# Optimization experiments

Hardware: AMD Instinct MI355X
Metric: run time of the kernel (lower is better)

The kernel has to match this reference:

```python
import jax, jax.numpy as jnp
import numpy as np

# Fixed by module source / config defaults
L, H, D, DFF, T, B = 4, 4, 128, 512, 64, 1024
S, V, BOS = 4, 5, 4            # 4 orbital states, vocab 5, BOS token id 4
DH = D // H


def _ln(x, w, b):
    mu = x.mean(-1, keepdims=True)
    var = ((x - mu) ** 2).mean(-1, keepdims=True)
    return (x - mu) / jnp.sqrt(var + 1e-5) * w + b


def _decode(gumbel, state_emb, pos_emb, ln1_w, ln1_b, wqkv, bqkv, wo, bo,
            ln2_w, ln2_b, w1, b1, w2, b2, fn_w, fn_b, head_w, head_b,
            n_alpha, n_beta):
    def step(carry, xs):
        tok, a_rem, b_rem, Kc, Vc = carry
        g, i = xs                                   # g: (B,4), i: step index
        x = state_emb[tok] + pos_emb[i]             # (B, D)
        for l in range(L):
            # pre-LN causal self-attention with KV cache (torch MHA math)
            xn = _ln(x, ln1_w[l], ln1_b[l])
            q, k, v = jnp.split(xn @ wqkv[l].T + bqkv[l], 3, axis=-1)
            Kc = Kc.at[l, :, i].set(k)
            Vc = Vc.at[l, :, i].set(v)
            qh = q.reshape(B, H, DH)
            kh = Kc[l].reshape(B, T, H, DH)
            vh = Vc[l].reshape(B, T, H, DH)
            sc = jnp.einsum('bhd,bthd->bht', qh, kh) / jnp.sqrt(jnp.float32(DH))
            sc = jnp.where((jnp.arange(T) <= i)[None, None, :], sc, -jnp.inf)
            ctx = jnp.einsum('bht,bthd->bhd', jax.nn.softmax(sc, -1), vh).reshape(B, D)
            x = x + ctx @ wo[l].T + bo[l]
            # pre-LN FFN (exact GELU, matching nn.GELU default)
            h = jax.nn.gelu(_ln(x, ln2_w[l], ln2_b[l]) @ w1[l].T + b1[l], approximate=False)
            x = x + h @ w2[l].T + b2[l]
        logits = _ln(x, fn_w, fn_b) @ head_w.T + head_b   # (B, 4)
        # electron-budget validity mask (compute_validity_mask)
        oa = T - i - 1
        m = jnp.stack([
            (a_rem <= oa) & (b_rem <= oa),
            (b_rem > 0) & (a_rem <= oa) & (b_rem - 1 <= oa),
            (a_rem > 0) & (a_rem - 1 <= oa) & (b_rem <= oa),
            (a_rem > 0) & (b_rem > 0) & (a_rem - 1 <= oa) & (b_rem - 1 <= oa)], -1)
        logp = jax.nn.log_softmax(jnp.where(m, logits, -jnp.inf), -1)
        s = jnp.argmax(logp + g, -1)                # gumbel-max == multinomial
        lp = jnp.take_along_axis(logp, s[:, None], 1)[:, 0]
        return (s, a_rem - (s >> 1), b_rem - (s & 1), Kc, Vc), (s, lp)

    tok0 = jnp.full((B,), BOS, jnp.int32)
    a0 = jnp.full((B,), n_alpha, jnp.int32)
    b0 = jnp.full((B,), n_beta, jnp.int32)
    Kc0 = jnp.zeros((L, B, T, D), jnp.float32)
    Vc0 = jnp.zeros((L, B, T, D), jnp.float32)
    _, (states, lps) = jax.lax.scan(
        step, (tok0, a0, b0, Kc0, Vc0), (gumbel.transpose(1, 0, 2), jnp.arange(T)))
    return states.T, lps.sum(0)                      # (B, T) states, (B,) log-prob


def setup_inputs() -> dict:
    key = jax.random.key(0)
    ks = jax.random.split(key, 10)
    p = lambda k, shp: jax.random.normal(k, shp, jnp.float32) * 0.02
    u = jax.random.uniform(ks[0], (B, T, S), jnp.float32, 1e-6, 1.0 - 1e-6)
    return {
        'gumbel': -jnp.log(-jnp.log(u)),
        'state_emb': p(ks[1], (V, D)),
        'pos_emb': p(ks[2], (T + 1, D)),
        'ln1_w': jnp.ones((L, D)), 'ln1_b': jnp.zeros((L, D)),
        'wqkv': p(ks[3], (L, 3 * D, D)), 'bqkv': jnp.zeros((L, 3 * D)),
        'wo': p(ks[4], (L, D, D)), 'bo': jnp.zeros((L, D)),
        'ln2_w': jnp.ones((L, D)), 'ln2_b': jnp.zeros((L, D)),
        'w1': p(ks[5], (L, DFF, D)), 'b1': jnp.zeros((L, DFF)),
        'w2': p(ks[6], (L, D, DFF)), 'b2': jnp.zeros((L, D)),
        'fn_w': jnp.ones((D,)), 'fn_b': jnp.zeros((D,)),
        'head_w': p(ks[7], (S, D)), 'head_b': jnp.zeros((S,)),
        'n_alpha': 16, 'n_beta': 16,
    }


def reference(gumbel, state_emb, pos_emb, ln1_w, ln1_b, wqkv, bqkv, wo, bo,
              ln2_w, ln2_b, w1, b1, w2, b2, fn_w, fn_b, head_w, head_b,
              n_alpha, n_beta):
    return _decode(gumbel, state_emb, pos_emb, ln1_w, ln1_b, wqkv, bqkv, wo, bo,
                   ln2_w, ln2_b, w1, b1, w2, b2, fn_w, fn_b, head_w, head_b,
                   n_alpha, n_beta)
```

## Files before the change

### kernel.cpp

```cpp
#include <hip/hip_runtime.h>
#include <math.h>

namespace {
constexpr int L_ = 4, H_ = 4, D_ = 128, DFF_ = 512, T_ = 64, B_ = 1024;
constexpr int S_ = 4, BOS_ = 4, DH_ = 32;
constexpr int NB = 4;
constexpr int NBLK = B_ / NB;
constexpr int NTH = 512;

constexpr size_t KC_BLK = (size_t)L_ * NB * T_ * D_;
constexpr size_t KC_OFF = 0;
constexpr size_t VC_OFF = KC_OFF + (size_t)NBLK * KC_BLK;
}

__device__ __forceinline__ float4 ld4(const float* p) {
  return *reinterpret_cast<const float4*>(p);
}

__device__ __forceinline__ float wredsum64(float v) {
#pragma unroll
  for (int off = 32; off > 0; off >>= 1) v += __shfl_xor(v, off, 64);
  return v;
}

__device__ __forceinline__ float gelu_exact(float v) {
  return 0.5f * v * (1.0f + erff(v * 0.70710678118654752440f));
}

__global__ __launch_bounds__(NTH) void decode_kernel(
    const float* __restrict__ gumbel, const float* __restrict__ state_emb,
    const float* __restrict__ pos_emb,
    const float* __restrict__ ln1w, const float* __restrict__ ln1b,
    const float* __restrict__ wqkv, const float* __restrict__ bqkv,
    const float* __restrict__ wo, const float* __restrict__ bo,
    const float* __restrict__ ln2w, const float* __restrict__ ln2b,
    const float* __restrict__ w1, const float* __restrict__ b1,
    const float* __restrict__ w2, const float* __restrict__ b2,
    const float* __restrict__ fnw, const float* __restrict__ fnb,
    const float* __restrict__ headw, const float* __restrict__ headb,
    const int* __restrict__ nalpha, const int* __restrict__ nbeta,
    float* __restrict__ ws, float* __restrict__ out) {
  const int tid = threadIdx.x;
  const int blk = blockIdx.x;
  const int lane = tid & 63;
  const int wv = tid >> 6;
  const int slot = tid >> 2;
  const int dq = tid & 3;

  float* Kc = ws + KC_OFF + (size_t)blk * KC_BLK;
  float* Vc = ws + VC_OFF + (size_t)blk * KC_BLK;

  __shared__ __align__(16) float xres[NB][D_];
  __shared__ __align__(16) float xn[NB][D_];
  __shared__ __align__(16) float qbuf[NB][3 * D_];
  __shared__ __align__(16) float hbuf[NB][DFF_];
  __shared__ float sc[NB][H_][T_];
  __shared__ float wred[NTH / 64];
  __shared__ float logits[NB][S_];
  __shared__ int tok[NB], arem[NB], brem[NB];
  __shared__ float lpsum[NB];

  if (tid < NB) {
    tok[tid] = BOS_;
    arem[tid] = nalpha[0];
    brem[tid] = nbeta[0];
    lpsum[tid] = 0.f;
  }
  __syncthreads();

  for (int i = 0; i < T_; ++i) {
    {
      const int e = tid >> 7, d = tid & 127;
      xres[e][d] = state_emb[tok[e] * D_ + d] + pos_emb[i * D_ + d];
    }
    __syncthreads();

    for (int l = 0; l < L_; ++l) {
      {
        const int e = tid >> 7, d = tid & 127;
        float v = xres[e][d];
        float s = wredsum64(v);
        if (lane == 0) wred[wv] = s;
        __syncthreads();
        float mu = (wred[2 * e] + wred[2 * e + 1]) * (1.f / 128.f);
        __syncthreads();
        float dv = v - mu;
        float s2 = wredsum64(dv * dv);
        if (lane == 0) wred[wv] = s2;
        __syncthreads();
        float var = (wred[2 * e] + wred[2 * e + 1]) * (1.f / 128.f);
        xn[e][d] = dv * (1.f / sqrtf(var + 1e-5f)) * ln1w[l * D_ + d] + ln1b[l * D_ + d];
      }
      __syncthreads();

      {
#pragma unroll
        for (int p = 0; p < 3; ++p) {
          const int o = p * 128 + slot;
          const float* wrow = wqkv + ((size_t)l * 384 + o) * D_;
          float a0 = 0.f, a1 = 0.f, a2 = 0.f, a3 = 0.f;
#pragma unroll
          for (int j = 0; j < 8; ++j) {
            const int d0 = 16 * j + 4 * dq;
            const float4 w4 = ld4(wrow + d0);
            const float4 x0 = ld4(&xn[0][d0]);
            const float4 x1 = ld4(&xn[1][d0]);
            const float4 x2 = ld4(&xn[2][d0]);
            const float4 x3 = ld4(&xn[3][d0]);
            a0 += w4.x * x0.x + w4.y * x0.y + w4.z * x0.z + w4.w * x0.w;
            a1 += w4.x * x1.x + w4.y * x1.y + w4.z * x1.z + w4.w * x1.w;
            a2 += w4.x * x2.x + w4.y * x2.y + w4.z * x2.z + w4.w * x2.w;
            a3 += w4.x * x3.x + w4.y * x3.y + w4.z * x3.z + w4.w * x3.w;
          }
          a0 += __shfl_xor(a0, 1); a0 += __shfl_xor(a0, 2);
          a1 += __shfl_xor(a1, 1); a1 += __shfl_xor(a1, 2);
          a2 += __shfl_xor(a2, 1); a2 += __shfl_xor(a2, 2);
          a3 += __shfl_xor(a3, 1); a3 += __shfl_xor(a3, 2);
          float r = (dq == 0) ? a0 : (dq == 1) ? a1 : (dq == 2) ? a2 : a3;
          qbuf[dq][o] = r + bqkv[l * 384 + o];
        }
      }
      __syncthreads();

      {
        const int e = tid >> 7, d = tid & 127;
        size_t base = (((size_t)l * NB + e) * T_ + i) * D_ + d;
        Kc[base] = qbuf[e][D_ + d];
        Vc[base] = qbuf[e][2 * D_ + d];
      }
      __syncthreads();

      {
        const int pid = tid >> 5, j = tid & 31;
        const int e = pid >> 2, h = pid & 3;
        const float4* q4 = reinterpret_cast<const float4*>(&qbuf[e][h * DH_]);
        for (int t = j; t <= i; t += 32) {
          const float4* kp = reinterpret_cast<const float4*>(
              Kc + (((size_t)l * NB + e) * T_ + t) * D_ + h * DH_);
          float acc = 0.f;
#pragma unroll
          for (int k = 0; k < 8; ++k) {
            float4 a = q4[k], bv = kp[k];
            acc += a.x * bv.x + a.y * bv.y + a.z * bv.z + a.w * bv.w;
          }
          sc[e][h][t] = acc * 0.17677669529663687f;
        }
      }
      __syncthreads();

      {
        const int pid = tid >> 5, j = tid & 31;
        const int e = pid >> 2, h = pid & 3;
        float m = -INFINITY;
        for (int t = j; t <= i; t += 32) m = fmaxf(m, sc[e][h][t]);
#pragma unroll
        for (int off = 16; off > 0; off >>= 1) m = fmaxf(m, __shfl_xor(m, off, 32));
        float sum = 0.f;
        for (int t = j; t <= i; t += 32) {
          float p = expf(sc[e][h][t] - m);
          sc[e][h][t] = p;
          sum += p;
        }
#pragma unroll
        for (int off = 16; off > 0; off >>= 1) sum += __shfl_xor(sum, off, 32);
        float inv = 1.f / sum;
        for (int t = j; t <= i; t += 32) sc[e][h][t] *= inv;
      }
      __syncthreads();

      {
        const int e = tid >> 7, d = tid & 127, h = d >> 5;
        const float* vp = Vc + (((size_t)l * NB + e) * T_) * D_ + d;
        const float* pw = &sc[e][h][0];
        float acc = 0.f;
        int t = 0;
        for (; t + 4 <= i + 1; t += 4) {
          acc += pw[t] * vp[(size_t)t * D_];
          acc += pw[t + 1] * vp[(size_t)(t + 1) * D_];
          acc += pw[t + 2] * vp[(size_t)(t + 2) * D_];
          acc += pw[t + 3] * vp[(size_t)(t + 3) * D_];
        }
        for (; t <= i; ++t) acc += pw[t] * vp[(size_t)t * D_];
        qbuf[e][d] = acc;
      }
      __syncthreads();

      {
        const int o = slot;
        const float* wrow = wo + ((size_t)l * 128 + o) * D_;
        float a0 = 0.f, a1 = 0.f, a2 = 0.f, a3 = 0.f;
#pragma unroll
        for (int j = 0; j < 8; ++j) {
          const int d0 = 16 * j + 4 * dq;
          const float4 w4 = ld4(wrow + d0);
          const float4 x0 = ld4(&qbuf[0][d0]);
          const float4 x1 = ld4(&qbuf[1][d0]);
          const float4 x2 = ld4(&qbuf[2][d0]);
          const float4 x3 = ld4(&qbuf[3][d0]);
          a0 += w4.x * x0.x + w4.y * x0.y + w4.z * x0.z + w4.w * x0.w;
          a1 += w4.x * x1.x + w4.y * x1.y + w4.z * x1.z + w4.w * x1.w;
          a2 += w4.x * x2.x + w4.y * x2.y + w4.z * x2.z + w4.w * x2.w;
          a3 += w4.x * x3.x + w4.y * x3.y + w4.z * x3.z + w4.w * x3.w;
        }
        a0 += __shfl_xor(a0, 1); a0 += __shfl_xor(a0, 2);
        a1 += __shfl_xor(a1, 1); a1 += __shfl_xor(a1, 2);
        a2 += __shfl_xor(a2, 1); a2 += __shfl_xor(a2, 2);
        a3 += __shfl_xor(a3, 1); a3 += __shfl_xor(a3, 2);
        float r = (dq == 0) ? a0 : (dq == 1) ? a1 : (dq == 2) ? a2 : a3;
        xres[dq][o] += r + bo[l * D_ + o];
      }
      __syncthreads();

      {
        const int e = tid >> 7, d = tid & 127;
        float v = xres[e][d];
        float s = wredsum64(v);
        if (lane == 0) wred[wv] = s;
        __syncthreads();
        float mu = (wred[2 * e] + wred[2 * e + 1]) * (1.f / 128.f);
        __syncthreads();
        float dv = v - mu;
        float s2 = wredsum64(dv * dv);
        if (lane == 0) wred[wv] = s2;
        __syncthreads();
        float var = (wred[2 * e] + wred[2 * e + 1]) * (1.f / 128.f);
        xn[e][d] = dv * (1.f / sqrtf(var + 1e-5f)) * ln2w[l * D_ + d] + ln2b[l * D_ + d];
      }
      __syncthreads();

      {
#pragma unroll
        for (int p = 0; p < 4; ++p) {
          const int o = p * 128 + slot;
          const float* wrow = w1 + ((size_t)l * DFF_ + o) * D_;
          float a0 = 0.f, a1 = 0.f, a2 = 0.f, a3 = 0.f;
#pragma unroll
          for (int j = 0; j < 8; ++j) {
            const int d0 = 16 * j + 4 * dq;
            const float4 w4 = ld4(wrow + d0);
            const float4 x0 = ld4(&xn[0][d0]);
            const float4 x1 = ld4(&xn[1][d0]);
            const float4 x2 = ld4(&xn[2][d0]);
            const float4 x3 = ld4(&xn[3][d0]);
            a0 += w4.x * x0.x + w4.y * x0.y + w4.z * x0.z + w4.w * x0.w;
            a1 += w4.x * x1.x + w4.y * x1.y + w4.z * x1.z + w4.w * x1.w;
            a2 += w4.x * x2.x + w4.y * x2.y + w4.z * x2.z + w4.w * x2.w;
            a3 += w4.x * x3.x + w4.y * x3.y + w4.z * x3.z + w4.w * x3.w;
          }
          a0 += __shfl_xor(a0, 1); a0 += __shfl_xor(a0, 2);
          a1 += __shfl_xor(a1, 1); a1 += __shfl_xor(a1, 2);
          a2 += __shfl_xor(a2, 1); a2 += __shfl_xor(a2, 2);
          a3 += __shfl_xor(a3, 1); a3 += __shfl_xor(a3, 2);
          float r = (dq == 0) ? a0 : (dq == 1) ? a1 : (dq == 2) ? a2 : a3;
          hbuf[dq][o] = gelu_exact(r + b1[l * DFF_ + o]);
        }
      }
      __syncthreads();

      {
        const int o = slot;
        const float* wrow = w2 + ((size_t)l * 128 + o) * DFF_;
        float a0 = 0.f, a1 = 0.f, a2 = 0.f, a3 = 0.f;
#pragma unroll 8
        for (int j = 0; j < 32; ++j) {
          const int d0 = 16 * j + 4 * dq;
          const float4 w4 = ld4(wrow + d0);
          const float4 x0 = ld4(&hbuf[0][d0]);
          const float4 x1 = ld4(&hbuf[1][d0]);
          const float4 x2 = ld4(&hbuf[2][d0]);
          const float4 x3 = ld4(&hbuf[3][d0]);
          a0 += w4.x * x0.x + w4.y * x0.y + w4.z * x0.z + w4.w * x0.w;
          a1 += w4.x * x1.x + w4.y * x1.y + w4.z * x1.z + w4.w * x1.w;
          a2 += w4.x * x2.x + w4.y * x2.y + w4.z * x2.z + w4.w * x2.w;
          a3 += w4.x * x3.x + w4.y * x3.y + w4.z * x3.z + w4.w * x3.w;
        }
        a0 += __shfl_xor(a0, 1); a0 += __shfl_xor(a0, 2);
        a1 += __shfl_xor(a1, 1); a1 += __shfl_xor(a1, 2);
        a2 += __shfl_xor(a2, 1); a2 += __shfl_xor(a2, 2);
        a3 += __shfl_xor(a3, 1); a3 += __shfl_xor(a3, 2);
        float r = (dq == 0) ? a0 : (dq == 1) ? a1 : (dq == 2) ? a2 : a3;
        xres[dq][o] += r + b2[l * D_ + o];
      }
      __syncthreads();
    }

    {
      const int e = tid >> 7, d = tid & 127;
      float v = xres[e][d];
      float s = wredsum64(v);
      if (lane == 0) wred[wv] = s;
      __syncthreads();
      float mu = (wred[2 * e] + wred[2 * e + 1]) * (1.f / 128.f);
      __syncthreads();
      float dv = v - mu;
      float s2 = wredsum64(dv * dv);
      if (lane == 0) wred[wv] = s2;
      __syncthreads();
      float var = (wred[2 * e] + wred[2 * e + 1]) * (1.f / 128.f);
      xn[e][d] = dv * (1.f / sqrtf(var + 1e-5f)) * fnw[d] + fnb[d];
    }
    __syncthreads();

    if (tid < 128) {
      const int e = tid >> 5, rest = tid & 31, s = rest >> 3, j = rest & 7;
      const float4* xv = reinterpret_cast<const float4*>(xn[e]);
      const float4* hw = reinterpret_cast<const float4*>(headw + s * D_);
      float acc = 0.f;
#pragma unroll
      for (int k = 4 * j; k < 4 * j + 4; ++k) {
        float4 a = xv[k], w = hw[k];
        acc += a.x * w.x + a.y * w.y + a.z * w.z + a.w * w.w;
      }
      acc += __shfl_xor(acc, 1);
      acc += __shfl_xor(acc, 2);
      acc += __shfl_xor(acc, 4);
      if (j == 0) logits[e][s] = acc + headb[s];
    }
    __syncthreads();

    if (tid < NB) {
      const int e = tid;
      const int b = blk * NB + e;
      int a = arem[e], bb = brem[e];
      int oa = T_ - 1 - i;
      bool m[4];
      m[0] = (a <= oa) && (bb <= oa);
      m[1] = (bb > 0) && (a <= oa) && (bb - 1 <= oa);
      m[2] = (a > 0) && (a - 1 <= oa) && (bb <= oa);
      m[3] = (a > 0) && (bb > 0) && (a - 1 <= oa) && (bb - 1 <= oa);
      float mx = -INFINITY;
#pragma unroll
      for (int s = 0; s < 4; ++s)
        if (m[s]) mx = fmaxf(mx, logits[e][s]);
      float sum = 0.f;
      float lg[4];
#pragma unroll
      for (int s = 0; s < 4; ++s) {
        if (m[s]) {
          float z = logits[e][s] - mx;
          sum += expf(z);
          lg[s] = z;
        } else {
          lg[s] = -INFINITY;
        }
      }
      float lse = logf(sum);
      float best = -INFINITY;
      int bs = 0;
#pragma unroll
      for (int s = 0; s < 4; ++s) {
        float lp = lg[s] - lse;
        float y = lp + gumbel[(size_t)b * T_ * S_ + (size_t)i * S_ + s];
        if (y > best) { best = y; bs = s; }
      }
      lpsum[e] += lg[bs] - lse;
      out[(size_t)b * T_ + i] = (float)bs;
      tok[e] = bs;
      arem[e] = a - (bs >> 1);
      brem[e] = bb - (bs & 1);
    }
    __syncthreads();
  }

  if (tid < NB) out[(size_t)B_ * T_ + (size_t)blk * NB + tid] = lpsum[tid];
}

extern "C" void kernel_launch(void* const* d_in, const int* in_sizes, int n_in,
                              void* d_out, int out_size, void* d_ws, size_t ws_size,
                              hipStream_t stream) {
  const float* gumbel    = (const float*)d_in[0];
  const float* state_emb = (const float*)d_in[1];
  const float* pos_emb   = (const float*)d_in[2];
  const float* ln1w      = (const float*)d_in[3];
  const float* ln1b      = (const float*)d_in[4];
  const float* wqkv      = (const float*)d_in[5];
  const float* bqkv      = (const float*)d_in[6];
  const float* wo        = (const float*)d_in[7];
  const float* bo        = (const float*)d_in[8];
  const float* ln2w      = (const float*)d_in[9];
  const float* ln2b      = (const float*)d_in[10];
  const float* w1        = (const float*)d_in[11];
  const float* b1        = (const float*)d_in[12];
  const float* w2        = (const float*)d_in[13];
  const float* b2        = (const float*)d_in[14];
  const float* fnw       = (const float*)d_in[15];
  const float* fnb       = (const float*)d_in[16];
  const float* headw     = (const float*)d_in[17];
  const float* headb     = (const float*)d_in[18];
  const int* nalpha      = (const int*)d_in[19];
  const int* nbeta       = (const int*)d_in[20];
  float* ws = (float*)d_ws;
  float* out = (float*)d_out;

  decode_kernel<<<dim3(NBLK), dim3(NTH), 0, stream>>>(
      gumbel, state_emb, pos_emb, ln1w, ln1b, wqkv, bqkv, wo, bo, ln2w, ln2b,
      w1, b1, w2, b2, fnw, fnb, headw, headb, nalpha, nbeta, ws, out);
}
```

Before: 7.932 ms.

## Cut block barriers: wave-local layernorm, fused attention, direct KV writes

Layernorm is now done by a single wave per sequence with shuffle reductions, so the cross-wave shared-memory reduction and its extra barriers are gone. The QKV projection writes K and V straight to the global cache, and the scores, softmax and normalisation are merged into one register-resident pass. V rows are prefetched into registers before the score phase and consumed by a 4-way split PV reduction. Matmul loops reuse the activation loads across output groups, and launch bounds ask for two blocks per CU. The cost is higher register pressure (16 float4 for V plus the accumulators), which may cause spills under the occupancy hint.

```diff
diff --git a/kernel.cpp b/kernel.cpp
--- a/kernel.cpp
+++ b/kernel.cpp
@@ -17,17 +17,29 @@
   return *reinterpret_cast<const float4*>(p);
 }
 
-__device__ __forceinline__ float wredsum64(float v) {
-#pragma unroll
-  for (int off = 32; off > 0; off >>= 1) v += __shfl_xor(v, off, 64);
-  return v;
-}
-
 __device__ __forceinline__ float gelu_exact(float v) {
   return 0.5f * v * (1.0f + erff(v * 0.70710678118654752440f));
 }
 
-__global__ __launch_bounds__(NTH) void decode_kernel(
+__device__ __forceinline__ void ln_wave(const float* __restrict__ src,
+                                        float* __restrict__ dst,
+                                        const float* __restrict__ w,
+                                        const float* __restrict__ b, int lane) {
+  float v0 = src[lane], v1 = src[lane + 64];
+  float s = v0 + v1;
+#pragma unroll
+  for (int off = 32; off > 0; off >>= 1) s += __shfl_xor(s, off);
+  float mu = s * (1.f / 128.f);
+  float d0 = v0 - mu, d1 = v1 - mu;
+  float s2 = d0 * d0 + d1 * d1;
+#pragma unroll
+  for (int off = 32; off > 0; off >>= 1) s2 += __shfl_xor(s2, off);
+  float inv = 1.f / sqrtf(s2 * (1.f / 128.f) + 1e-5f);
+  dst[lane] = d0 * inv * w[lane] + b[lane];
+  dst[lane + 64] = d1 * inv * w[lane + 64] + b[lane + 64];
+}
+
+__global__ __launch_bounds__(NTH, 2) void decode_kernel(
     const float* __restrict__ gumbel, const float* __restrict__ state_emb,
     const float* __restrict__ pos_emb,
     const float* __restrict__ ln1w, const float* __restrict__ ln1b,
@@ -52,10 +64,9 @@
 
   __shared__ __align__(16) float xres[NB][D_];
   __shared__ __align__(16) float xn[NB][D_];
-  __shared__ __align__(16) float qbuf[NB][3 * D_];
+  __shared__ __align__(16) float qbuf[NB][D_];
   __shared__ __align__(16) float hbuf[NB][DFF_];
-  __shared__ float sc[NB][H_][T_];
-  __shared__ float wred[NTH / 64];
+  __shared__ __align__(16) float sc[NB][H_][T_];
   __shared__ float logits[NB][S_];
   __shared__ int tok[NB], arem[NB], brem[NB];
   __shared__ float lpsum[NB];
@@ -68,6 +79,10 @@
   }
   __syncthreads();
 
+  const int ce = slot >> 5;
+  const int cc = slot & 31;
+  const int ch = cc >> 3;
+
   for (int i = 0; i < T_; ++i) {
     {
       const int e = tid >> 7, d = tid & 127;
@@ -76,118 +91,125 @@
     __syncthreads();
 
     for (int l = 0; l < L_; ++l) {
-      {
-        const int e = tid >> 7, d = tid & 127;
-        float v = xres[e][d];
-        float s = wredsum64(v);
-        if (lane == 0) wred[wv] = s;
-        __syncthreads();
-        float mu = (wred[2 * e] + wred[2 * e + 1]) * (1.f / 128.f);
-        __syncthreads();
-        float dv = v - mu;
-        float s2 = wredsum64(dv * dv);
-        if (lane == 0) wred[wv] = s2;
-        __syncthreads();
-        float var = (wred[2 * e] + wred[2 * e + 1]) * (1.f / 128.f);
-        xn[e][d] = dv * (1.f / sqrtf(var + 1e-5f)) * ln1w[l * D_ + d] + ln1b[l * D_ + d];
-      }
-      __syncthreads();
-
-      {
+      if (wv < NB) ln_wave(xres[wv], xn[wv], ln1w + l * D_, ln1b + l * D_, lane);
+      __syncthreads();
+
+      {
+        float acc[3][4];
+#pragma unroll
+        for (int p = 0; p < 3; ++p)
+#pragma unroll
+          for (int e = 0; e < 4; ++e) acc[p][e] = 0.f;
+        const float* wbase = wqkv + ((size_t)l * 384 + slot) * D_;
+#pragma unroll
+        for (int j = 0; j < 8; ++j) {
+          const int d0 = 16 * j + 4 * dq;
+          float4 xv[4];
+#pragma unroll
+          for (int e = 0; e < 4; ++e) xv[e] = ld4(&xn[e][d0]);
+#pragma unroll
+          for (int p = 0; p < 3; ++p) {
+            const float4 w4 = ld4(wbase + (size_t)(p * 128) * D_ + d0);
+#pragma unroll
+            for (int e = 0; e < 4; ++e) {
+              acc[p][e] += w4.x * xv[e].x + w4.y * xv[e].y +
+                           w4.z * xv[e].z + w4.w * xv[e].w;
+            }
+          }
+        }
 #pragma unroll
         for (int p = 0; p < 3; ++p) {
-          const int o = p * 128 + slot;
-          const float* wrow = wqkv + ((size_t)l * 384 + o) * D_;
-          float a0 = 0.f, a1 = 0.f, a2 = 0.f, a3 = 0.f;
-#pragma unroll
-          for (int j = 0; j < 8; ++j) {
-            const int d0 = 16 * j + 4 * dq;
-            const float4 w4 = ld4(wrow + d0);
-            const float4 x0 = ld4(&xn[0][d0]);
-            const float4 x1 = ld4(&xn[1][d0]);
-            const float4 x2 = ld4(&xn[2][d0]);
-            const float4 x3 = ld4(&xn[3][d0]);
-            a0 += w4.x * x0.x + w4.y * x0.y + w4.z * x0.z + w4.w * x0.w;
-            a1 += w4.x * x1.x + w4.y * x1.y + w4.z * x1.z + w4.w * x1.w;
-            a2 += w4.x * x2.x + w4.y * x2.y + w4.z * x2.z + w4.w * x2.w;
-            a3 += w4.x * x3.x + w4.y * x3.y + w4.z * x3.z + w4.w * x3.w;
-          }
-          a0 += __shfl_xor(a0, 1); a0 += __shfl_xor(a0, 2);
-          a1 += __shfl_xor(a1, 1); a1 += __shfl_xor(a1, 2);
-          a2 += __shfl_xor(a2, 1); a2 += __shfl_xor(a2, 2);
-          a3 += __shfl_xor(a3, 1); a3 += __shfl_xor(a3, 2);
-          float r = (dq == 0) ? a0 : (dq == 1) ? a1 : (dq == 2) ? a2 : a3;
-          qbuf[dq][o] = r + bqkv[l * 384 + o];
-        }
-      }
-      __syncthreads();
-
-      {
-        const int e = tid >> 7, d = tid & 127;
-        size_t base = (((size_t)l * NB + e) * T_ + i) * D_ + d;
-        Kc[base] = qbuf[e][D_ + d];
-        Vc[base] = qbuf[e][2 * D_ + d];
-      }
-      __syncthreads();
-
-      {
+#pragma unroll
+          for (int e = 0; e < 4; ++e) {
+            acc[p][e] += __shfl_xor(acc[p][e], 1);
+            acc[p][e] += __shfl_xor(acc[p][e], 2);
+          }
+          float r = (dq == 0) ? acc[p][0] : (dq == 1) ? acc[p][1]
+                   : (dq == 2) ? acc[p][2] : acc[p][3];
+          r += bqkv[l * 384 + p * 128 + slot];
+          if (p == 0) {
+            qbuf[dq][slot] = r;
+          } else if (p == 1) {
+            Kc[(((size_t)l * NB + dq) * T_ + i) * D_ + slot] = r;
+          } else {
+            Vc[(((size_t)l * NB + dq) * T_ + i) * D_ + slot] = r;
+          }
+        }
+      }
+      __syncthreads();
+
+      float4 vreg[16];
+      {
+        const float* vpb = Vc + ((size_t)l * NB + ce) * T_ * D_ + cc * 4;
+#pragma unroll
+        for (int jj = 0; jj < 16; ++jj) {
+          const int t = 4 * jj + dq;
+          if (t <= i) vreg[jj] = ld4(vpb + (size_t)t * D_);
+        }
         const int pid = tid >> 5, j = tid & 31;
         const int e = pid >> 2, h = pid & 3;
         const float4* q4 = reinterpret_cast<const float4*>(&qbuf[e][h * DH_]);
-        for (int t = j; t <= i; t += 32) {
-          const float4* kp = reinterpret_cast<const float4*>(
-              Kc + (((size_t)l * NB + e) * T_ + t) * D_ + h * DH_);
-          float acc = 0.f;
+        const float* kb = Kc + ((size_t)l * NB + e) * T_ * D_ + h * DH_;
+        float s0 = -INFINITY, s1 = -INFINITY;
+        if (j <= i) {
+          const float4* kp = reinterpret_cast<const float4*>(kb + (size_t)j * D_);
+          float a = 0.f;
 #pragma unroll
           for (int k = 0; k < 8; ++k) {
-            float4 a = q4[k], bv = kp[k];
-            acc += a.x * bv.x + a.y * bv.y + a.z * bv.z + a.w * bv.w;
-          }
-          sc[e][h][t] = acc * 0.17677669529663687f;
-        }
-      }
-      __syncthreads();
-
-      {
-        const int pid = tid >> 5, j = tid & 31;
-        const int e = pid >> 2, h = pid & 3;
-        float m = -INFINITY;
-        for (int t = j; t <= i; t += 32) m = fmaxf(m, sc[e][h][t]);
+            float4 qv = q4[k], kv = kp[k];
+            a += qv.x * kv.x + qv.y * kv.y + qv.z * kv.z + qv.w * kv.w;
+          }
+          s0 = a * 0.17677669529663687f;
+        }
+        if (j + 32 <= i) {
+          const float4* kp = reinterpret_cast<const float4*>(kb + (size_t)(j + 32) * D_);
+          float a = 0.f;
+#pragma unroll
+          for (int k = 0; k < 8; ++k) {
+            float4 qv = q4[k], kv = kp[k];
+            a += qv.x * kv.x + qv.y * kv.y + qv.z * kv.z + qv.w * kv.w;
+          }
+          s1 = a * 0.17677669529663687f;
+        }
+        float m = fmaxf(s0, s1);
 #pragma unroll
         for (int off = 16; off > 0; off >>= 1) m = fmaxf(m, __shfl_xor(m, off, 32));
-        float sum = 0.f;
-        for (int t = j; t <= i; t += 32) {
-          float p = expf(sc[e][h][t] - m);
-          sc[e][h][t] = p;
-          sum += p;
-        }
+        float p0 = expf(s0 - m), p1 = expf(s1 - m);
+        float sum = p0 + p1;
 #pragma unroll
         for (int off = 16; off > 0; off >>= 1) sum += __shfl_xor(sum, off, 32);
         float inv = 1.f / sum;
-        for (int t = j; t <= i; t += 32) sc[e][h][t] *= inv;
-      }
-      __syncthreads();
-
-      {
-        const int e = tid >> 7, d = tid & 127, h = d >> 5;
-        const float* vp = Vc + (((size_t)l * NB + e) * T_) * D_ + d;
-        const float* pw = &sc[e][h][0];
-        float acc = 0.f;
-        int t = 0;
-        for (; t + 4 <= i + 1; t += 4) {
-          acc += pw[t] * vp[(size_t)t * D_];
-          acc += pw[t + 1] * vp[(size_t)(t + 1) * D_];
-          acc += pw[t + 2] * vp[(size_t)(t + 2) * D_];
-          acc += pw[t + 3] * vp[(size_t)(t + 3) * D_];
-        }
-        for (; t <= i; ++t) acc += pw[t] * vp[(size_t)t * D_];
-        qbuf[e][d] = acc;
-      }
-      __syncthreads();
-
-      {
-        const int o = slot;
-        const float* wrow = wo + ((size_t)l * 128 + o) * D_;
+        sc[e][h][j] = p0 * inv;
+        sc[e][h][j + 32] = p1 * inv;
+      }
+      __syncthreads();
+
+      {
+        float ax = 0.f, ay = 0.f, az = 0.f, aw = 0.f;
+#pragma unroll
+        for (int jj = 0; jj < 16; ++jj) {
+          const int t = 4 * jj + dq;
+          if (t <= i) {
+            const float p = sc[ce][ch][t];
+            ax += p * vreg[jj].x;
+            ay += p * vreg[jj].y;
+            az += p * vreg[jj].z;
+            aw += p * vreg[jj].w;
+          }
+        }
+        ax += __shfl_xor(ax, 1); ax += __shfl_xor(ax, 2);
+        ay += __shfl_xor(ay, 1); ay += __shfl_xor(ay, 2);
+        az += __shfl_xor(az, 1); az += __shfl_xor(az, 2);
+        aw += __shfl_xor(aw, 1); aw += __shfl_xor(aw, 2);
+        if (dq == 0) {
+          float4 r = {ax, ay, az, aw};
+          *reinterpret_cast<float4*>(&qbuf[ce][cc * 4]) = r;
+        }
+      }
+      __syncthreads();
+
+      {
+        const float* wrow = wo + ((size_t)l * 128 + slot) * D_;
         float a0 = 0.f, a1 = 0.f, a2 = 0.f, a3 = 0.f;
 #pragma unroll
         for (int j = 0; j < 8; ++j) {
@@ -207,61 +229,54 @@
         a2 += __shfl_xor(a2, 1); a2 += __shfl_xor(a2, 2);
         a3 += __shfl_xor(a3, 1); a3 += __shfl_xor(a3, 2);
         float r = (dq == 0) ? a0 : (dq == 1) ? a1 : (dq == 2) ? a2 : a3;
-        xres[dq][o] += r + bo[l * D_ + o];
-      }
-      __syncthreads();
-
-      {
-        const int e = tid >> 7, d = tid & 127;
-        float v = xres[e][d];
-        float s = wredsum64(v);
-        if (lane == 0) wred[wv] = s;
-        __syncthreads();
-        float mu = (wred[2 * e] + wred[2 * e + 1]) * (1.f / 128.f);
-        __syncthreads();
-        float dv = v - mu;
-        float s2 = wredsum64(dv * dv);
-        if (lane == 0) wred[wv] = s2;
-        __syncthreads();
-        float var = (wred[2 * e] + wred[2 * e + 1]) * (1.f / 128.f);
-        xn[e][d] = dv * (1.f / sqrtf(var + 1e-5f)) * ln2w[l * D_ + d] + ln2b[l * D_ + d];
-      }
-      __syncthreads();
-
-      {
+        xres[dq][slot] += r + bo[l * D_ + slot];
+      }
+      __syncthreads();
+
+      if (wv < NB) ln_wave(xres[wv], xn[wv], ln2w + l * D_, ln2b + l * D_, lane);
+      __syncthreads();
+
+      {
+        float acc[4][4];
+#pragma unroll
+        for (int p = 0; p < 4; ++p)
+#pragma unroll
+          for (int e = 0; e < 4; ++e) acc[p][e] = 0.f;
+        const float* wbase = w1 + ((size_t)l * DFF_ + slot) * D_;
+#pragma unroll
+        for (int j = 0; j < 8; ++j) {
+          const int d0 = 16 * j + 4 * dq;
+          float4 xv[4];
+#pragma unroll
+          for (int e = 0; e < 4; ++e) xv[e] = ld4(&xn[e][d0]);
+#pragma unroll
+          for (int p = 0; p < 4; ++p) {
+            const float4 w4 = ld4(wbase + (size_t)(p * 128) * D_ + d0);
+#pragma unroll
+            for (int e = 0; e < 4; ++e) {
+              acc[p][e] += w4.x * xv[e].x + w4.y * xv[e].y +
+                           w4.z * xv[e].z + w4.w * xv[e].w;
+            }
+          }
+        }
 #pragma unroll
         for (int p = 0; p < 4; ++p) {
-          const int o = p * 128 + slot;
-          const float* wrow = w1 + ((size_t)l * DFF_ + o) * D_;
-          float a0 = 0.f, a1 = 0.f, a2 = 0.f, a3 = 0.f;
-#pragma unroll
-          for (int j = 0; j < 8; ++j) {
-            const int d0 = 16 * j + 4 * dq;
-            const float4 w4 = ld4(wrow + d0);
-            const float4 x0 = ld4(&xn[0][d0]);
-            const float4 x1 = ld4(&xn[1][d0]);
-            const float4 x2 = ld4(&xn[2][d0]);
-            const float4 x3 = ld4(&xn[3][d0]);
-            a0 += w4.x * x0.x + w4.y * x0.y + w4.z * x0.z + w4.w * x0.w;
-            a1 += w4.x * x1.x + w4.y * x1.y + w4.z * x1.z + w4.w * x1.w;
-            a2 += w4.x * x2.x + w4.y * x2.y + w4.z * x2.z + w4.w * x2.w;
-            a3 += w4.x * x3.x + w4.y * x3.y + w4.z * x3.z + w4.w * x3.w;
-          }
-          a0 += __shfl_xor(a0, 1); a0 += __shfl_xor(a0, 2);
-          a1 += __shfl_xor(a1, 1); a1 += __shfl_xor(a1, 2);
-          a2 += __shfl_xor(a2, 1); a2 += __shfl_xor(a2, 2);
-          a3 += __shfl_xor(a3, 1); a3 += __shfl_xor(a3, 2);
-          float r = (dq == 0) ? a0 : (dq == 1) ? a1 : (dq == 2) ? a2 : a3;
-          hbuf[dq][o] = gelu_exact(r + b1[l * DFF_ + o]);
-        }
-      }
-      __syncthreads();
-
-      {
-        const int o = slot;
-        const float* wrow = w2 + ((size_t)l * 128 + o) * DFF_;
+#pragma unroll
+          for (int e = 0; e < 4; ++e) {
+            acc[p][e] += __shfl_xor(acc[p][e], 1);
+            acc[p][e] += __shfl_xor(acc[p][e], 2);
+          }
+          float r = (dq == 0) ? acc[p][0] : (dq == 1) ? acc[p][1]
+                   : (dq == 2) ? acc[p][2] : acc[p][3];
+          hbuf[dq][p * 128 + slot] = gelu_exact(r + b1[l * DFF_ + p * 128 + slot]);
+        }
+      }
+      __syncthreads();
+
+      {
+        const float* wrow = w2 + ((size_t)l * 128 + slot) * DFF_;
         float a0 = 0.f, a1 = 0.f, a2 = 0.f, a3 = 0.f;
-#pragma unroll 8
+#pragma unroll
         for (int j = 0; j < 32; ++j) {
           const int d0 = 16 * j + 4 * dq;
           const float4 w4 = ld4(wrow + d0);
@@ -279,26 +294,12 @@
         a2 += __shfl_xor(a2, 1); a2 += __shfl_xor(a2, 2);
         a3 += __shfl_xor(a3, 1); a3 += __shfl_xor(a3, 2);
         float r = (dq == 0) ? a0 : (dq == 1) ? a1 : (dq == 2) ? a2 : a3;
-        xres[dq][o] += r + b2[l * D_ + o];
+        xres[dq][slot] += r + b2[l * D_ + slot];
       }
       __syncthreads();
     }
 
-    {
-      const int e = tid >> 7, d = tid & 127;
-      float v = xres[e][d];
-      float s = wredsum64(v);
-      if (lane == 0) wred[wv] = s;
-      __syncthreads();
-      float mu = (wred[2 * e] + wred[2 * e + 1]) * (1.f / 128.f);
-      __syncthreads();
-      float dv = v - mu;
-      float s2 = wredsum64(dv * dv);
-      if (lane == 0) wred[wv] = s2;
-      __syncthreads();
-      float var = (wred[2 * e] + wred[2 * e + 1]) * (1.f / 128.f);
-      xn[e][d] = dv * (1.f / sqrtf(var + 1e-5f)) * fnw[d] + fnb[d];
-    }
+    if (wv < NB) ln_wave(xres[wv], xn[wv], fnw, fnb, lane);
     __syncthreads();
 
     if (tid < 128) {
```

After: 10.36 ms. 30.6% more time.
